# Performance work log

Measured on AMD Instinct MI355X. Metric: run time of the kernel, lower is better.

## Reference

```python
import jax, jax.numpy as jnp
import numpy as np

T, B, D, W = 1024, 8, 512, 32

def setup_inputs() -> dict:
    key = jax.random.key(0)
    k1, k2, k3 = jax.random.split(key, 3)
    inputs = jax.random.normal(k1, (T, B, D), dtype=jnp.float32)
    weight_W = jax.random.uniform(k2, (D, D), dtype=jnp.float32, minval=-0.1, maxval=0.1)
    weight_proj = jax.random.uniform(k3, (D, 1), dtype=jnp.float32, minval=-0.1, maxval=0.1)
    return {"inputs": inputs, "weight_W": weight_W, "weight_proj": weight_proj,
            "attention_width": W}

def reference(inputs, weight_W, weight_proj, attention_width):
    # inputs: [T, B, D]. For step i < w: passthrough. For i >= w: attend over
    # window inputs[i-w : i] (current step EXCLUDED, matching the original).
    Tn, Bn, Dn = inputs.shape
    w = attention_width
    # window gather indices: row t corresponds to output step i = t + w,
    # covering timesteps [i-w, i) == [t, t+w)
    idx = jnp.arange(Tn - w)[:, None] + jnp.arange(w)          # [T-w, w]
    windows = inputs[idx]                                       # [T-w, w, B, D]
    u = jnp.tanh(jnp.einsum('twbd,de->twbe', windows, weight_W))  # [T-w, w, B, D]
    scores = jnp.einsum('twbd,d->twb', u, weight_proj[:, 0])      # [T-w, w, B]
    # NOTE: original uses legacy nn.Softmax() on a [w, B] tensor, whose implicit
    # dim is 1 (the batch dim). We reproduce that math faithfully: softmax over B.
    a = jax.nn.softmax(scores, axis=-1)                           # [T-w, w, B]
    attended = jnp.einsum('twb,twbd->tbd', a, windows)            # [T-w, B, D]
    return jnp.concatenate([inputs[:w], attended], axis=0)       # [T, B, D]
```

## Files before the change

kernel.cpp:

```cpp
#include <hip/hip_runtime.h>
#include <cstdint>

namespace {
constexpr int T = 1024;
constexpr int B = 8;
constexpr int D = 512;
constexpr int W = 32;
constexpr int M = T * B;
}

using half8  = __attribute__((ext_vector_type(8))) _Float16;
using f32x16 = __attribute__((ext_vector_type(16))) float;

__device__ __forceinline__ void gload16(const void* g, void* l) {
    __builtin_amdgcn_global_load_lds(
        (const __attribute__((address_space(1))) void*)g,
        (__attribute__((address_space(3))) void*)l, 16, 0, 0);
}

__device__ __forceinline__ float fast_tanh(float x) {
    float e = __expf(2.f * x);
    return 1.f - 2.f / (e + 1.f);
}

__global__ __launch_bounds__(256) void prep_merged(
    const float* __restrict__ X, const float* __restrict__ Wm,
    _Float16* __restrict__ Ah, _Float16* __restrict__ Bt)
{
    __shared__ float tile[64][65];
    const int tid = threadIdx.x;
    const int bid = blockIdx.x;

    {
        const int c = bid * 256 + tid;
        const float4* X4 = reinterpret_cast<const float4*>(X);
        const float4 v0 = X4[(size_t)c * 2];
        const float4 v1 = X4[(size_t)c * 2 + 1];
        half8 h;
        h[0] = (_Float16)v0.x; h[1] = (_Float16)v0.y; h[2] = (_Float16)v0.z; h[3] = (_Float16)v0.w;
        h[4] = (_Float16)v1.x; h[5] = (_Float16)v1.y; h[6] = (_Float16)v1.z; h[7] = (_Float16)v1.w;
        *reinterpret_cast<half8*>(Ah + (size_t)c * 8) = h;
    }

    if (bid < 64) {
        const int bd = bid & 7;
        const int be = bid >> 3;
        const int r  = tid >> 2;
        const int c0 = (tid & 3) * 16;
        const float* src = Wm + (size_t)(be * 64 + r) * 512 + bd * 64 + c0;
#pragma unroll
        for (int j = 0; j < 16; j += 4) {
            const float4 v = *reinterpret_cast<const float4*>(src + j);
            tile[r][c0 + j]     = v.x;
            tile[r][c0 + j + 1] = v.y;
            tile[r][c0 + j + 2] = v.z;
            tile[r][c0 + j + 3] = v.w;
        }
        __syncthreads();
        const int dd = tid >> 2;
        const int e0 = (tid & 3) * 16;
        half8 h0, h1;
#pragma unroll
        for (int j = 0; j < 8; ++j)  h0[j] = (_Float16)tile[e0 + j][dd];
#pragma unroll
        for (int j = 0; j < 8; ++j)  h1[j] = (_Float16)tile[e0 + 8 + j][dd];
        _Float16* dst = Bt + (size_t)(bd * 64 + dd) * 512 + be * 64 + e0;
        *reinterpret_cast<half8*>(dst)     = h0;
        *reinterpret_cast<half8*>(dst + 8) = h1;
    }
}

__global__ __launch_bounds__(256) void gemm_scores(
    const _Float16* __restrict__ Ah, const _Float16* __restrict__ Bt,
    const float* __restrict__ proj, float* __restrict__ spart)
{
    __shared__ char lds_buf[65536];

    const int tid  = threadIdx.x;
    const int lane = tid & 63;
    const int wv   = tid >> 6;
    const int wm   = wv >> 1;
    const int wn   = wv & 1;
    const int hi   = lane >> 5;
    const int l31  = lane & 31;
    const int l7   = lane & 7;

    const int bid  = blockIdx.x;
    const int wgid = (bid & 7) * 32 + (bid >> 3);
    const int mb   = wgid >> 2;
    const int nb   = wgid & 3;
    const int m0   = mb * 128;
    const int n0   = nb * 128;

    const int wbase = __builtin_amdgcn_readfirstlane(tid & ~63);

    f32x16 acc00 = {}, acc01 = {}, acc10 = {}, acc11 = {};

    auto stage = [&](int bufi, int kt) {
        char* abase = lds_buf + bufi * 32768;
        char* bbase = abase + 16384;
        const int kbase = kt * 64;
#pragma unroll
        for (int i = 0; i < 4; ++i) {
            const int c   = i * 256 + tid;
            const int row = c >> 3;
            const int ch  = c & 7;
            const int koff = kbase + ((ch ^ (row & 7)) << 3);
            gload16(Ah + (size_t)(m0 + row) * 512 + koff,
                    abase + (size_t)(i * 256 + wbase) * 16);
            gload16(Bt + (size_t)(n0 + row) * 512 + koff,
                    bbase + (size_t)(i * 256 + wbase) * 16);
        }
    };

    stage(0, 0);
    asm volatile("s_waitcnt vmcnt(0)" ::: "memory");
    __syncthreads();

    int cur = 0;
    const int rowA0 = wm * 64 + l31;
    const int rowA1 = rowA0 + 32;
    const int colB0 = wn * 64 + l31;
    const int colB1 = colB0 + 32;

    for (int kt = 0; kt < 8; ++kt) {
        if (kt < 7) stage(cur ^ 1, kt + 1);

        const char* Ab = lds_buf + cur * 32768;
        const char* Bb = Ab + 16384;

        half8 af0[4], af1[4], bf0[4], bf1[4];
#pragma unroll
        for (int s = 0; s < 4; ++s) {
            const int ch = ((2 * s + hi) ^ l7) << 4;
            af0[s] = *reinterpret_cast<const half8*>(Ab + rowA0 * 128 + ch);
            af1[s] = *reinterpret_cast<const half8*>(Ab + rowA1 * 128 + ch);
            bf0[s] = *reinterpret_cast<const half8*>(Bb + colB0 * 128 + ch);
            bf1[s] = *reinterpret_cast<const half8*>(Bb + colB1 * 128 + ch);
        }
        __builtin_amdgcn_s_setprio(1);
#pragma unroll
        for (int s = 0; s < 4; ++s) {
            acc00 = __builtin_amdgcn_mfma_f32_32x32x16_f16(af0[s], bf0[s], acc00, 0, 0, 0);
            acc01 = __builtin_amdgcn_mfma_f32_32x32x16_f16(af0[s], bf1[s], acc01, 0, 0, 0);
            acc10 = __builtin_amdgcn_mfma_f32_32x32x16_f16(af1[s], bf0[s], acc10, 0, 0, 0);
            acc11 = __builtin_amdgcn_mfma_f32_32x32x16_f16(af1[s], bf1[s], acc11, 0, 0, 0);
        }
        __builtin_amdgcn_s_setprio(0);

        if (kt < 7) asm volatile("s_waitcnt vmcnt(0)" ::: "memory");
        __syncthreads();
        cur ^= 1;
    }

    const float pj0 = proj[n0 + wn * 64 + l31];
    const float pj1 = proj[n0 + wn * 64 + 32 + l31];
    float* sp = spart + (size_t)(nb * 2 + wn) * M;

#pragma unroll
    for (int reg = 0; reg < 16; ++reg) {
        float v0 = fast_tanh(acc00[reg]) * pj0 + fast_tanh(acc01[reg]) * pj1;
        float v1 = fast_tanh(acc10[reg]) * pj0 + fast_tanh(acc11[reg]) * pj1;
#pragma unroll
        for (int msk = 1; msk < 32; msk <<= 1) {
            v0 += __shfl_xor(v0, msk, 64);
            v1 += __shfl_xor(v1, msk, 64);
        }
        if (l31 == 0) {
            const int rl = (reg & 3) + 8 * (reg >> 2) + 4 * hi;
            const int m  = m0 + wm * 64 + rl;
            sp[m]      = v0;
            sp[m + 32] = v1;
        }
    }
}

__global__ __launch_bounds__(256) void attend_kernel(
    const float* __restrict__ X, const float* __restrict__ spart,
    float* __restrict__ out)
{
    __shared__ float sm[35][8];
    __shared__ float p_lds[35];

    const int bid  = blockIdx.x;
    const int b    = bid & 7;
    const int ig   = bid >> 3;
    const int tid  = threadIdx.x;
    const int rg   = tid >> 6;
    const int lane = tid & 63;
    const int i    = ig * 4 + rg;

    const float4* X4 = reinterpret_cast<const float4*>(X);
    float4* O4       = reinterpret_cast<float4*>(out);
    const size_t obase = (size_t)(i * B + b) * (D / 4) + lane * 2;

    if (ig < 8) {
        O4[obase]     = X4[obase];
        O4[obase + 1] = X4[obase + 1];
        return;
    }

    const int tau0 = ig * 4 - 32;
    for (int idx = tid; idx < 35 * 8; idx += 256) {
        const int tj = idx >> 3;
        const int bj = idx & 7;
        float s = 0.f;
#pragma unroll
        for (int g = 0; g < 8; ++g)
            s += spart[(size_t)g * M + (size_t)(tau0 + tj) * 8 + bj];
        sm[tj][bj] = s;
    }
    __syncthreads();
    if (tid < 35) {
        float v[8];
#pragma unroll
        for (int j = 0; j < 8; ++j) v[j] = sm[tid][j];
        float mx = v[0];
#pragma unroll
        for (int j = 1; j < 8; ++j) mx = fmaxf(mx, v[j]);
        float sum = 0.f;
#pragma unroll
        for (int j = 0; j < 8; ++j) { v[j] = __expf(v[j] - mx); sum += v[j]; }
        p_lds[tid] = v[b] / sum;
    }
    __syncthreads();

    float4 a0 = {0.f, 0.f, 0.f, 0.f}, a1 = {0.f, 0.f, 0.f, 0.f};
#pragma unroll 4
    for (int k = 0; k < W; ++k) {
        const int tau  = i - W + k;
        const float pw = p_lds[rg + k];
        const size_t rbase = (size_t)(tau * B + b) * (D / 4) + lane * 2;
        const float4 v0 = X4[rbase];
        const float4 v1 = X4[rbase + 1];
        a0.x = fmaf(pw, v0.x, a0.x); a0.y = fmaf(pw, v0.y, a0.y);
        a0.z = fmaf(pw, v0.z, a0.z); a0.w = fmaf(pw, v0.w, a0.w);
        a1.x = fmaf(pw, v1.x, a1.x); a1.y = fmaf(pw, v1.y, a1.y);
        a1.z = fmaf(pw, v1.z, a1.z); a1.w = fmaf(pw, v1.w, a1.w);
    }
    O4[obase]     = a0;
    O4[obase + 1] = a1;
}

extern "C" void kernel_launch(void* const* d_in, const int* in_sizes, int n_in,
                              void* d_out, int out_size, void* d_ws, size_t ws_size,
                              hipStream_t stream)
{
    const float* X    = (const float*)d_in[0];
    const float* Wm   = (const float*)d_in[1];
    const float* proj = (const float*)d_in[2];
    float* out = (float*)d_out;

    _Float16* Ah   = (_Float16*)d_ws;
    _Float16* Bt   = Ah + (size_t)M * D;
    float*    sprt = (float*)(Bt + (size_t)D * D);

    prep_merged<<<2048, 256, 0, stream>>>(X, Wm, Ah, Bt);
    gemm_scores<<<256, 256, 0, stream>>>(Ah, Bt, proj, sprt);
    attend_kernel<<<(T / 4) * B, 256, 0, stream>>>(X, sprt, out);
}
```

Measured before the change: 43.39 us.

## Stage fp16 window rows in LDS and compute 32 outputs per block

The attend kernel now handles 32 output timesteps per block instead of 4. It loads the 63 needed fp16 input rows into LDS once with async global-to-LDS copies and reuses them across all 32 outputs, which cuts repeated global reads of the overlapping windows. The per-row softmax over batch now uses wave shuffles instead of a separate LDS pass. In exchange the weighted sum reads the fp16 copy rather than the fp32 input, which lowers precision, and the large LDS footprint with only 256 blocks reduces occupancy.

```diff
diff --git a/kernel.cpp b/kernel.cpp
--- a/kernel.cpp
+++ b/kernel.cpp
@@ -176,70 +176,102 @@
 }
 
 __global__ __launch_bounds__(256) void attend_kernel(
-    const float* __restrict__ X, const float* __restrict__ spart,
-    float* __restrict__ out)
-{
-    __shared__ float sm[35][8];
-    __shared__ float p_lds[35];
-
-    const int bid  = blockIdx.x;
-    const int b    = bid & 7;
-    const int ig   = bid >> 3;
-    const int tid  = threadIdx.x;
-    const int rg   = tid >> 6;
+    const float* __restrict__ X, const _Float16* __restrict__ Ah,
+    const float* __restrict__ spart, float* __restrict__ out)
+{
+    __shared__ _Float16 W_lds[63 * 512];
+    __shared__ float p_lds[64];
+
+    const int bid = blockIdx.x;
+    const int b   = bid & 7;
+    const int ig  = bid >> 3;
+    const int tid = threadIdx.x;
+
+    if (ig == 0) {
+        const float4* X4 = reinterpret_cast<const float4*>(X);
+        float4* O4 = reinterpret_cast<float4*>(out);
+        for (int idx = tid; idx < 32 * 128; idx += 256) {
+            const int r = idx >> 7;
+            const int c = idx & 127;
+            const size_t off = (size_t)(r * 8 + b) * 128 + c;
+            O4[off] = X4[off];
+        }
+        return;
+    }
+
+    const int i0   = ig * 32;
+    const int tau0 = i0 - 32;
     const int lane = tid & 63;
-    const int i    = ig * 4 + rg;
-
-    const float4* X4 = reinterpret_cast<const float4*>(X);
-    float4* O4       = reinterpret_cast<float4*>(out);
-    const size_t obase = (size_t)(i * B + b) * (D / 4) + lane * 2;
-
-    if (ig < 8) {
-        O4[obase]     = X4[obase];
-        O4[obase + 1] = X4[obase + 1];
-        return;
-    }
-
-    const int tau0 = ig * 4 - 32;
-    for (int idx = tid; idx < 35 * 8; idx += 256) {
-        const int tj = idx >> 3;
-        const int bj = idx & 7;
-        float s = 0.f;
-#pragma unroll
-        for (int g = 0; g < 8; ++g)
-            s += spart[(size_t)g * M + (size_t)(tau0 + tj) * 8 + bj];
-        sm[tj][bj] = s;
-    }
+    const int wbase = __builtin_amdgcn_readfirstlane(tid & ~63);
+
+    {
+        const _Float16* src = Ah + (size_t)(tau0 * 8 + b) * 512;
+#pragma unroll
+        for (int it = 0; it < 16; ++it) {
+            const int cbase = it * 256 + wbase;
+            if (cbase < 4032) {
+                const int c  = cbase + lane;
+                const int r  = c >> 6;
+                const int ch = c & 63;
+                gload16(src + (size_t)r * 4096 + ch * 8,
+                        (char*)W_lds + (size_t)cbase * 16);
+            }
+        }
+    }
+
+    const int bj = tid & 7;
+#pragma unroll
+    for (int half = 0; half < 2; ++half) {
+        const int lt = (tid >> 3) + half * 32;
+        if (lt < 63) {
+            float s = 0.f;
+#pragma unroll
+            for (int g = 0; g < 8; ++g)
+                s += spart[(size_t)g * M + (size_t)(tau0 + lt) * 8 + bj];
+            float mx = s;
+#pragma unroll
+            for (int msk = 1; msk < 8; msk <<= 1)
+                mx = fmaxf(mx, __shfl_xor(mx, msk, 64));
+            const float e = __expf(s - mx);
+            float sum = e;
+#pragma unroll
+            for (int msk = 1; msk < 8; msk <<= 1)
+                sum += __shfl_xor(sum, msk, 64);
+            if (bj == b) p_lds[lt] = e / sum;
+        }
+    }
+
+    asm volatile("s_waitcnt vmcnt(0)" ::: "memory");
     __syncthreads();
-    if (tid < 35) {
-        float v[8];
-#pragma unroll
-        for (int j = 0; j < 8; ++j) v[j] = sm[tid][j];
-        float mx = v[0];
-#pragma unroll
-        for (int j = 1; j < 8; ++j) mx = fmaxf(mx, v[j]);
-        float sum = 0.f;
-#pragma unroll
-        for (int j = 0; j < 8; ++j) { v[j] = __expf(v[j] - mx); sum += v[j]; }
-        p_lds[tid] = v[b] / sum;
-    }
-    __syncthreads();
-
-    float4 a0 = {0.f, 0.f, 0.f, 0.f}, a1 = {0.f, 0.f, 0.f, 0.f};
+
+    const int rg = tid >> 6;
+
+#pragma unroll 2
+    for (int q = 0; q < 8; ++q) {
+        const int i  = i0 + rg * 8 + q;
+        const int lb = rg * 8 + q;
+        float a0 = 0.f, a1 = 0.f, a2 = 0.f, a3 = 0.f;
+        float a4 = 0.f, a5 = 0.f, a6 = 0.f, a7 = 0.f;
 #pragma unroll 4
-    for (int k = 0; k < W; ++k) {
-        const int tau  = i - W + k;
-        const float pw = p_lds[rg + k];
-        const size_t rbase = (size_t)(tau * B + b) * (D / 4) + lane * 2;
-        const float4 v0 = X4[rbase];
-        const float4 v1 = X4[rbase + 1];
-        a0.x = fmaf(pw, v0.x, a0.x); a0.y = fmaf(pw, v0.y, a0.y);
-        a0.z = fmaf(pw, v0.z, a0.z); a0.w = fmaf(pw, v0.w, a0.w);
-        a1.x = fmaf(pw, v1.x, a1.x); a1.y = fmaf(pw, v1.y, a1.y);
-        a1.z = fmaf(pw, v1.z, a1.z); a1.w = fmaf(pw, v1.w, a1.w);
-    }
-    O4[obase]     = a0;
-    O4[obase + 1] = a1;
+        for (int k = 0; k < 32; ++k) {
+            const int lt = lb + k;
+            const float pw = p_lds[lt];
+            const half8 h = *reinterpret_cast<const half8*>(
+                W_lds + (size_t)lt * 512 + lane * 8);
+            a0 = fmaf(pw, (float)h[0], a0);
+            a1 = fmaf(pw, (float)h[1], a1);
+            a2 = fmaf(pw, (float)h[2], a2);
+            a3 = fmaf(pw, (float)h[3], a3);
+            a4 = fmaf(pw, (float)h[4], a4);
+            a5 = fmaf(pw, (float)h[5], a5);
+            a6 = fmaf(pw, (float)h[6], a6);
+            a7 = fmaf(pw, (float)h[7], a7);
+        }
+        float4* O4 = reinterpret_cast<float4*>(
+            out + (size_t)(i * 8 + b) * 512 + lane * 8);
+        O4[0] = float4{a0, a1, a2, a3};
+        O4[1] = float4{a4, a5, a6, a7};
+    }
 }
 
 extern "C" void kernel_launch(void* const* d_in, const int* in_sizes, int n_in,
@@ -257,5 +289,5 @@
 
     prep_merged<<<2048, 256, 0, stream>>>(X, Wm, Ah, Bt);
     gemm_scores<<<256, 256, 0, stream>>>(Ah, Bt, proj, sprt);
-    attend_kernel<<<(T / 4) * B, 256, 0, stream>>>(X, sprt, out);
-}
+    attend_kernel<<<(T / W) * B, 256, 0, stream>>>(X, Ah, sprt, out);
+}
```

Result: faster. 41.28 us (-4.9%).
